# Performance work log

Hardware: AMD Instinct MI355X
Metric: run time of the kernel (lower is better)

## Reference

```python
import jax, jax.numpy as jnp
import numpy as np

EMBED = 256
HEADS = 8
LEVELS = 3
POINTS = 4
MLP = 4
SS = np.array([[100, 100], [50, 50], [25, 25]], np.int32)  # (H, W) per level


def setup_inputs() -> dict:
    key = jax.random.key(0)
    ks = jax.random.split(key, 12)
    B, Q = 2, 128 * 128
    NV = int((SS[:, 0] * SS[:, 1]).sum())
    C = EMBED
    F = C * MLP
    s = 0.02

    def w(k, shape):
        return jax.random.normal(k, shape, jnp.float32) * s

    return dict(
        query=jax.random.normal(ks[0], (B, Q, C), jnp.float32),
        value=jax.random.normal(ks[1], (B, NV, C), jnp.float32),
        query_pos=jax.random.normal(ks[2], (B, Q, C), jnp.float32),
        ref_pts=jax.random.uniform(ks[3], (B, Q, 2), jnp.float32),
        spatial_shapes=SS,
        level_start_index=np.concatenate([[0], np.cumsum(SS[:, 0] * SS[:, 1])[:-1]]).astype(np.int32),
        ln1_g=jnp.ones(C), ln1_b=jnp.zeros(C),
        ln2_g=jnp.ones(C), ln2_b=jnp.zeros(C),
        W_value=w(ks[4], (C, C)), b_value=jnp.zeros(C),
        W_off=w(ks[5], (C, HEADS * LEVELS * POINTS * 2)), b_off=w(ks[6], (HEADS * LEVELS * POINTS * 2,)),
        W_attn=w(ks[7], (C, HEADS * LEVELS * POINTS)), b_attn=jnp.zeros(HEADS * LEVELS * POINTS),
        W_out=w(ks[8], (C, C)), b_out=jnp.zeros(C),
        W_ffn1=w(ks[9], (C, F)), b_ffn1=jnp.zeros(F),
        W_ffn2=w(ks[10], (F, C)), b_ffn2=jnp.zeros(C),
    )


def _layernorm(x, g, b, eps=1e-5):
    m = x.mean(-1, keepdims=True)
    v = ((x - m) ** 2).mean(-1, keepdims=True)
    return (x - m) * jax.lax.rsqrt(v + eps) * g + b


def _bilinear(v, loc, Hl, Wl):
    # v: [BH, Hl*Wl, d]; loc: [BH, Q, P, 2] normalized to [0,1].
    # grid_sample(align_corners=False, padding=zeros): pixel = loc*size - 0.5
    BH, Q, P, _ = loc.shape
    d = v.shape[-1]
    x = loc[..., 0] * Wl - 0.5
    y = loc[..., 1] * Hl - 0.5
    x0f = jnp.floor(x)
    y0f = jnp.floor(y)
    lx = x - x0f
    ly = y - y0f
    x0 = x0f.astype(jnp.int32)
    y0 = y0f.astype(jnp.int32)

    def gather(xi, yi):
        valid = ((xi >= 0) & (xi < Wl) & (yi >= 0) & (yi < Hl)).astype(v.dtype)
        idx = jnp.clip(yi, 0, Hl - 1) * Wl + jnp.clip(xi, 0, Wl - 1)
        g = jnp.take_along_axis(v, idx.reshape(BH, Q * P, 1), axis=1).reshape(BH, Q, P, d)
        return g * valid[..., None]

    w00 = (1 - lx) * (1 - ly)
    w01 = lx * (1 - ly)
    w10 = (1 - lx) * ly
    w11 = lx * ly
    return (gather(x0, y0) * w00[..., None] + gather(x0 + 1, y0) * w01[..., None]
            + gather(x0, y0 + 1) * w10[..., None] + gather(x0 + 1, y0 + 1) * w11[..., None])


def _forward(query, value, query_pos, ref_pts, spatial_shapes,
             ln1_g, ln1_b, ln2_g, ln2_b,
             W_value, b_value, W_off, b_off, W_attn, b_attn, W_out, b_out,
             W_ffn1, b_ffn1, W_ffn2, b_ffn2):
    B, Q, C = query.shape
    Hh, L, P = HEADS, LEVELS, POINTS
    d = C // Hh
    ss = np.asarray(spatial_shapes)
    starts = np.concatenate([[0], np.cumsum(ss[:, 0] * ss[:, 1])])

    # pre-norm + positional embedding (MSDeformAttn adds query_pos)
    qn = _layernorm(query, ln1_g, ln1_b)
    q = qn + query_pos

    # value projection, split heads
    v = (value @ W_value + b_value).reshape(B, -1, Hh, d)

    off = (q @ W_off + b_off).reshape(B, Q, Hh, L, P, 2)
    aw = jax.nn.softmax((q @ W_attn + b_attn).reshape(B, Q, Hh, L * P), axis=-1)
    aw = aw.reshape(B, Q, Hh, L, P)

    # offset normalizer is (W, H) per level
    normalizer = jnp.asarray(ss[:, ::-1].copy(), jnp.float32)
    # bev_value path: ref_pts broadcast over levels
    loc = ref_pts[:, :, None, None, None, :] + off / normalizer[None, None, None, :, None, :]

    out = jnp.zeros((B * Hh, Q, d), query.dtype)
    for l in range(L):
        Hl, Wl = int(ss[l, 0]), int(ss[l, 1])
        v_l = v[:, starts[l]:starts[l + 1]].transpose(0, 2, 1, 3).reshape(B * Hh, Hl * Wl, d)
        loc_l = loc[:, :, :, l].transpose(0, 2, 1, 3, 4).reshape(B * Hh, Q, P, 2)
        sampled = _bilinear(v_l, loc_l, Hl, Wl)  # [BH, Q, P, d]
        w_l = aw[:, :, :, l].transpose(0, 2, 1, 3).reshape(B * Hh, Q, P)
        out = out + (sampled * w_l[..., None]).sum(2)

    out = out.reshape(B, Hh, Q, d).transpose(0, 2, 1, 3).reshape(B, Q, C)
    x = query + (out @ W_out + b_out)

    h = _layernorm(x, ln2_g, ln2_b)
    x = x + (jax.nn.gelu(h @ W_ffn1 + b_ffn1, approximate=False) @ W_ffn2 + b_ffn2)
    return x


def reference(query, value, query_pos, ref_pts, spatial_shapes, level_start_index,
              ln1_g, ln1_b, ln2_g, ln2_b,
              W_value, b_value, W_off, b_off, W_attn, b_attn, W_out, b_out,
              W_ffn1, b_ffn1, W_ffn2, b_ffn2):
    return _forward(query, value, query_pos, ref_pts, spatial_shapes,
                    ln1_g, ln1_b, ln2_g, ln2_b,
                    W_value, b_value, W_off, b_off, W_attn, b_attn, W_out, b_out,
                    W_ffn1, b_ffn1, W_ffn2, b_ffn2)
```

## Files before the change

### kernel.cpp

```cpp
#include <hip/hip_runtime.h>
#include <hip/hip_bf16.h>

#define BQ      2
#define QLEN    16384
#define CDIM    256
#define HEADS   8
#define LEV     3
#define PTS     4
#define DHEAD   32
#define NVTOT   13125
#define FDIM    1024
#define NTOK    (BQ*QLEN)
#define MROWS_V (BQ*NVTOT)
#define NPROJ   288

typedef __attribute__((ext_vector_type(8))) short short8;
typedef __attribute__((ext_vector_type(4))) float floatx4;

typedef const __attribute__((address_space(1))) unsigned int gu32;
typedef __attribute__((address_space(3))) unsigned int lu32;

struct bf16x4 { __hip_bfloat16 v[4]; };

__device__ __forceinline__ int imin(int a, int b){ return a<b?a:b; }
__device__ __forceinline__ int imax(int a, int b){ return a>b?a:b; }

__device__ __forceinline__ float gelu_f(float x)
{
    float u = 0.7978845608028654f * (x + 0.044715f * x * x * x);
    float e = __expf(2.0f * u);
    float th = 1.0f - 2.0f / (e + 1.0f);
    return 0.5f * x * (1.0f + th);
}

__global__ __launch_bounds__(256)
void ln_bf16_k(const float* __restrict__ x, const float* __restrict__ pos,
               const float* __restrict__ g, const float* __restrict__ b,
               __hip_bfloat16* __restrict__ out)
{
    int tok  = blockIdx.x * 4 + (threadIdx.x >> 6);
    int lane = threadIdx.x & 63;
    float4 v = ((const float4*)(x + (size_t)tok * CDIM))[lane];
    float s = v.x + v.y + v.z + v.w;
    #pragma unroll
    for (int o = 32; o > 0; o >>= 1) s += __shfl_down(s, o);
    s = __shfl(s, 0);
    float mean = s * (1.0f / 256.0f);
    float4 c; c.x = v.x - mean; c.y = v.y - mean; c.z = v.z - mean; c.w = v.w - mean;
    float q2 = c.x*c.x + c.y*c.y + c.z*c.z + c.w*c.w;
    #pragma unroll
    for (int o = 32; o > 0; o >>= 1) q2 += __shfl_down(q2, o);
    q2 = __shfl(q2, 0);
    float rstd = rsqrtf(q2 * (1.0f / 256.0f) + 1e-5f);
    float4 gg = ((const float4*)g)[lane];
    float4 bb = ((const float4*)b)[lane];
    float4 o4;
    o4.x = c.x * rstd * gg.x + bb.x;
    o4.y = c.y * rstd * gg.y + bb.y;
    o4.z = c.z * rstd * gg.z + bb.z;
    o4.w = c.w * rstd * gg.w + bb.w;
    if (pos) {
        float4 p = ((const float4*)(pos + (size_t)tok * CDIM))[lane];
        o4.x += p.x; o4.y += p.y; o4.z += p.z; o4.w += p.w;
    }
    bf16x4 r;
    r.v[0] = __float2bfloat16(o4.x); r.v[1] = __float2bfloat16(o4.y);
    r.v[2] = __float2bfloat16(o4.z); r.v[3] = __float2bfloat16(o4.w);
    ((bf16x4*)(out + (size_t)tok * CDIM))[lane] = r;
}

__global__ __launch_bounds__(256)
void cvt_k(const float* __restrict__ in, __hip_bfloat16* __restrict__ out, int n4)
{
    int i = blockIdx.x * 256 + threadIdx.x;
    if (i >= n4) return;
    float4 v = ((const float4*)in)[i];
    bf16x4 r;
    r.v[0] = __float2bfloat16(v.x); r.v[1] = __float2bfloat16(v.y);
    r.v[2] = __float2bfloat16(v.z); r.v[3] = __float2bfloat16(v.w);
    ((bf16x4*)out)[i] = r;
}

__global__ __launch_bounds__(256)
void wt_all_k(const float* __restrict__ Wv,  const float* __restrict__ Woff,
              const float* __restrict__ Wat, const float* __restrict__ Wout,
              const float* __restrict__ W1,  const float* __restrict__ W2,
              const float* __restrict__ boff, const float* __restrict__ bat,
              __hip_bfloat16* __restrict__ o_v,  __hip_bfloat16* __restrict__ o_c,
              __hip_bfloat16* __restrict__ o_out,
              __hip_bfloat16* __restrict__ o_1,  __hip_bfloat16* __restrict__ o_2,
              float* __restrict__ o_bc)
{
    int gid = blockIdx.x * 256 + threadIdx.x;
    if (gid < 65536) {
        int idx = gid, n = idx >> 8, k = idx & 255;
        o_v[idx] = __float2bfloat16(Wv[(size_t)k * 256 + n]);
    } else if (gid < 163840) {
        int idx = gid - 65536, n = idx >> 8, k = idx & 255;
        float v = 0.0f;
        if (n < 192)       v = Woff[(size_t)k * 192 + n];
        else if (n < 288)  v = Wat[(size_t)k * 96 + (n - 192)];
        o_c[idx] = __float2bfloat16(v);
    } else if (gid < 229376) {
        int idx = gid - 163840, n = idx >> 8, k = idx & 255;
        o_out[idx] = __float2bfloat16(Wout[(size_t)k * 256 + n]);
    } else if (gid < 491520) {
        int idx = gid - 229376, n = idx >> 8, k = idx & 255;
        o_1[idx] = __float2bfloat16(W1[(size_t)k * 1024 + n]);
    } else if (gid < 753664) {
        int idx = gid - 491520, n = idx >> 10, k = idx & 1023;
        o_2[idx] = __float2bfloat16(W2[(size_t)k * 256 + n]);
    } else if (gid < 753952) {
        int idx = gid - 753664;
        o_bc[idx] = (idx < 192) ? boff[idx] : bat[idx - 192];
    }
}

enum { EP_PLAIN = 0, EP_VSCAT_BF16 = 1, EP_RES = 2, EP_GELU_BF16 = 3 };

__global__ __launch_bounds__(256)
void mm_k(const __hip_bfloat16* __restrict__ A, const __hip_bfloat16* __restrict__ Bt,
          const float* __restrict__ bias, const float* __restrict__ res,
          void* __restrict__ Cout, int M, int N, int K, int mode)
{
    __shared__ __hip_bfloat16 Ws[128 * 64];
    __shared__ __hip_bfloat16 Ts[128 * 64];
    int t = threadIdx.x;
    int lane = t & 63;
    int wave = t >> 6;
    int wm = wave >> 1, wn = wave & 1;
    int lm = lane & 15, lk = lane >> 4;
    int m0 = blockIdx.x * 128;
    int n0 = blockIdx.y * 128;

    floatx4 acc[4][4];
    #pragma unroll
    for (int i = 0; i < 4; i++)
        #pragma unroll
        for (int j = 0; j < 4; j++) acc[i][j] = (floatx4)0.0f;

    for (int kt = 0; kt < K; kt += 64) {
        #pragma unroll
        for (int i = 0; i < 4; i++) {
            int cc  = i * 256 + t;
            int row = cc >> 3;
            int c   = cc & 7;
            int kc  = c ^ (row & 7);
            int ra  = m0 + row; if (ra >= M) ra = M - 1;
            const __hip_bfloat16* gw = Bt + (size_t)(n0 + row) * K + kt + kc * 8;
            const __hip_bfloat16* gt = A  + (size_t)ra * K + kt + kc * 8;
            __builtin_amdgcn_global_load_lds((gu32*)gw, (lu32*)(Ws + cc * 8), 16, 0, 0);
            __builtin_amdgcn_global_load_lds((gu32*)gt, (lu32*)(Ts + cc * 8), 16, 0, 0);
        }
        __syncthreads();
        #pragma unroll
        for (int ks = 0; ks < 2; ks++) {
            short8 wf[4], tf[4];
            #pragma unroll
            for (int i = 0; i < 4; i++) {
                int rw = wn * 64 + i * 16 + lm;
                int cw = (ks * 4 + lk) ^ (rw & 7);
                wf[i] = *(const short8*)(Ws + (rw * 8 + cw) * 8);
                int rt = wm * 64 + i * 16 + lm;
                int ct = (ks * 4 + lk) ^ (rt & 7);
                tf[i] = *(const short8*)(Ts + (rt * 8 + ct) * 8);
            }
            #pragma unroll
            for (int i = 0; i < 4; i++)
                #pragma unroll
                for (int j = 0; j < 4; j++)
                    acc[i][j] = __builtin_amdgcn_mfma_f32_16x16x32_bf16(wf[i], tf[j], acc[i][j], 0, 0, 0);
        }
        __syncthreads();
    }

    #pragma unroll
    for (int i = 0; i < 4; i++) {
        int chan = n0 + wn * 64 + i * 16 + lk * 4;
        float4 b4 = make_float4(0.f, 0.f, 0.f, 0.f);
        if (chan < N) b4 = *(const float4*)(bias + chan);
        #pragma unroll
        for (int j = 0; j < 4; j++) {
            int tok = m0 + wm * 64 + j * 16 + lm;
            if (tok >= M || chan >= N) continue;
            float4 v;
            v.x = acc[i][j][0] + b4.x;
            v.y = acc[i][j][1] + b4.y;
            v.z = acc[i][j][2] + b4.z;
            v.w = acc[i][j][3] + b4.w;
            if (mode == EP_PLAIN) {
                *(float4*)((float*)Cout + (size_t)tok * N + chan) = v;
            } else if (mode == EP_VSCAT_BF16) {
                int bb  = tok / NVTOT;
                int pix = tok - bb * NVTOT;
                int hh  = chan >> 5, dc = chan & 31;
                bf16x4 r;
                r.v[0] = __float2bfloat16(v.x); r.v[1] = __float2bfloat16(v.y);
                r.v[2] = __float2bfloat16(v.z); r.v[3] = __float2bfloat16(v.w);
                *(bf16x4*)((__hip_bfloat16*)Cout
                    + (((size_t)(bb * HEADS + hh)) * NVTOT + pix) * DHEAD + dc) = r;
            } else if (mode == EP_RES) {
                float4 rr = *(const float4*)(res + (size_t)tok * N + chan);
                v.x += rr.x; v.y += rr.y; v.z += rr.z; v.w += rr.w;
                *(float4*)((float*)Cout + (size_t)tok * N + chan) = v;
            } else {
                bf16x4 r;
                r.v[0] = __float2bfloat16(gelu_f(v.x));
                r.v[1] = __float2bfloat16(gelu_f(v.y));
                r.v[2] = __float2bfloat16(gelu_f(v.z));
                r.v[3] = __float2bfloat16(gelu_f(v.w));
                *(bf16x4*)((__hip_bfloat16*)Cout + (size_t)tok * N + chan) = r;
            }
        }
    }
}

__global__ __launch_bounds__(256)
void sample_k(const __hip_bfloat16* __restrict__ v, const float* __restrict__ cbuf,
              const float* __restrict__ ref, __hip_bfloat16* __restrict__ out)
{
    __shared__ int4   metaIdx[4 * 104];
    __shared__ float4 metaW[4 * 104];

    int wid  = threadIdx.x >> 6;
    int lane = threadIdx.x & 63;
    int t    = blockIdx.x * 4 + wid;
    int b    = t >> 14;
    float rx = ref[(size_t)t * 2 + 0];
    float ry = ref[(size_t)t * 2 + 1];
    const float* crow = cbuf + (size_t)t * NPROJ;

    #pragma unroll
    for (int rnd = 0; rnd < 2; rnd++) {
        int slot = rnd * 64 + lane;
        int h = slot >> 4, p = slot & 15;
        int pc = imin(p, 11);
        float2 oxy  = *(const float2*)(crow + h * 24 + pc * 2);
        float logit = crow[192 + h * 12 + pc];
        float mx = logit;
        #pragma unroll
        for (int o = 8; o > 0; o >>= 1) mx = fmaxf(mx, __shfl_xor(mx, o, 16));
        float e = (p < 12) ? __expf(logit - mx) : 0.0f;
        float ssum = e;
        #pragma unroll
        for (int o = 8; o > 0; o >>= 1) ssum += __shfl_xor(ssum, o, 16);
        float aw = e / ssum;

        if (p < 12) {
            int l = p >> 2;
            float fS = (l == 0) ? 100.0f : ((l == 1) ? 50.0f : 25.0f);
            int   Wl = (l == 0) ? 100 : ((l == 1) ? 50 : 25);
            int   st = (l == 0) ? 0 : ((l == 1) ? 10000 : 12500);
            float x = (rx + oxy.x / fS) * fS - 0.5f;
            float y = (ry + oxy.y / fS) * fS - 0.5f;
            float x0f = floorf(x), y0f = floorf(y);
            float fx = x - x0f, fy = y - y0f;
            int x0 = (int)x0f, y0 = (int)y0f;
            int x1 = x0 + 1,  y1 = y0 + 1;
            int cx0 = imin(imax(x0, 0), Wl - 1), cx1 = imin(imax(x1, 0), Wl - 1);
            int cy0 = imin(imax(y0, 0), Wl - 1), cy1 = imin(imax(y1, 0), Wl - 1);
            float vx0 = (x0 >= 0 && x0 < Wl) ? 1.0f : 0.0f;
            float vx1 = (x1 >= 0 && x1 < Wl) ? 1.0f : 0.0f;
            float vy0 = (y0 >= 0 && y0 < Wl) ? 1.0f : 0.0f;
            float vy1 = (y1 >= 0 && y1 < Wl) ? 1.0f : 0.0f;
            int s = wid * 104 + h * 13 + p;
            metaIdx[s] = make_int4(st + cy0 * Wl + cx0, st + cy0 * Wl + cx1,
                                   st + cy1 * Wl + cx0, st + cy1 * Wl + cx1);
            metaW[s] = make_float4((1.0f - fx) * (1.0f - fy) * aw * vx0 * vy0,
                                   fx * (1.0f - fy) * aw * vx1 * vy0,
                                   (1.0f - fx) * fy * aw * vx0 * vy1,
                                   fx * fy * aw * vx1 * vy1);
        }
    }
    __syncthreads();

    int h  = lane >> 3;
    int c8 = lane & 7;
    const __hip_bfloat16* vbh = v + ((size_t)(b * HEADS + h)) * NVTOT * DHEAD + c8 * 4;
    float4 acc = {0.0f, 0.0f, 0.0f, 0.0f};
    #pragma unroll
    for (int p = 0; p < 12; p++) {
        int s = wid * 104 + h * 13 + p;
        int4   mi = metaIdx[s];
        float4 mw = metaW[s];
        ushort4 r0 = *(const ushort4*)(vbh + (size_t)mi.x * DHEAD);
        ushort4 r1 = *(const ushort4*)(vbh + (size_t)mi.y * DHEAD);
        ushort4 r2 = *(const ushort4*)(vbh + (size_t)mi.z * DHEAD);
        ushort4 r3 = *(const ushort4*)(vbh + (size_t)mi.w * DHEAD);
        acc.x = fmaf(mw.x, __uint_as_float((unsigned)r0.x << 16), acc.x);
        acc.y = fmaf(mw.x, __uint_as_float((unsigned)r0.y << 16), acc.y);
        acc.z = fmaf(mw.x, __uint_as_float((unsigned)r0.z << 16), acc.z);
        acc.w = fmaf(mw.x, __uint_as_float((unsigned)r0.w << 16), acc.w);
        acc.x = fmaf(mw.y, __uint_as_float((unsigned)r1.x << 16), acc.x);
        acc.y = fmaf(mw.y, __uint_as_float((unsigned)r1.y << 16), acc.y);
        acc.z = fmaf(mw.y, __uint_as_float((unsigned)r1.z << 16), acc.z);
        acc.w = fmaf(mw.y, __uint_as_float((unsigned)r1.w << 16), acc.w);
        acc.x = fmaf(mw.z, __uint_as_float((unsigned)r2.x << 16), acc.x);
        acc.y = fmaf(mw.z, __uint_as_float((unsigned)r2.y << 16), acc.y);
        acc.z = fmaf(mw.z, __uint_as_float((unsigned)r2.z << 16), acc.z);
        acc.w = fmaf(mw.z, __uint_as_float((unsigned)r2.w << 16), acc.w);
        acc.x = fmaf(mw.w, __uint_as_float((unsigned)r3.x << 16), acc.x);
        acc.y = fmaf(mw.w, __uint_as_float((unsigned)r3.y << 16), acc.y);
        acc.z = fmaf(mw.w, __uint_as_float((unsigned)r3.z << 16), acc.z);
        acc.w = fmaf(mw.w, __uint_as_float((unsigned)r3.w << 16), acc.w);
    }
    bf16x4 r;
    r.v[0] = __float2bfloat16(acc.x); r.v[1] = __float2bfloat16(acc.y);
    r.v[2] = __float2bfloat16(acc.z); r.v[3] = __float2bfloat16(acc.w);
    *(bf16x4*)(out + (size_t)t * CDIM + h * DHEAD + c8 * 4) = r;
}

extern "C" void kernel_launch(void* const* d_in, const int* in_sizes, int n_in,
                              void* d_out, int out_size, void* d_ws, size_t ws_size,
                              hipStream_t stream)
{
    const float* query = (const float*)d_in[0];
    const float* value = (const float*)d_in[1];
    const float* qpos  = (const float*)d_in[2];
    const float* ref   = (const float*)d_in[3];
    const float* ln1g  = (const float*)d_in[6];
    const float* ln1b  = (const float*)d_in[7];
    const float* ln2g  = (const float*)d_in[8];
    const float* ln2b  = (const float*)d_in[9];
    const float* Wv    = (const float*)d_in[10];
    const float* bv    = (const float*)d_in[11];
    const float* Woff  = (const float*)d_in[12];
    const float* boff  = (const float*)d_in[13];
    const float* Wat   = (const float*)d_in[14];
    const float* bat   = (const float*)d_in[15];
    const float* Wout  = (const float*)d_in[16];
    const float* bout  = (const float*)d_in[17];
    const float* W1    = (const float*)d_in[18];
    const float* b1    = (const float*)d_in[19];
    const float* W2    = (const float*)d_in[20];
    const float* b2    = (const float*)d_in[21];
    float* out = (float*)d_out;
    char*  ws  = (char*)d_ws;

    const size_t MB = 1024 * 1024;
    __hip_bfloat16* Wvt   = (__hip_bfloat16*)(ws + 0);
    __hip_bfloat16* Wct   = (__hip_bfloat16*)(ws + 131072);
    __hip_bfloat16* Woutt = (__hip_bfloat16*)(ws + 327680);
    __hip_bfloat16* W1t   = (__hip_bfloat16*)(ws + 458752);
    __hip_bfloat16* W2t   = (__hip_bfloat16*)(ws + 983040);
    float*          bcomb = (float*)(ws + 1507328);
    __hip_bfloat16* qbf   = (__hip_bfloat16*)(ws + 2  * MB);
    __hip_bfloat16* aoutb = (__hip_bfloat16*)(ws + 19 * MB);
    __hip_bfloat16* vbf   = (__hip_bfloat16*)(ws + 36 * MB);
    __hip_bfloat16* vbuf  = (__hip_bfloat16*)(ws + 50 * MB);
    float*          cbuf  = (float*)(ws + 77 * MB);
    __hip_bfloat16* gbf   = (__hip_bfloat16*)(ws + 50 * MB);
    __hip_bfloat16* hbf   = qbf;

    wt_all_k<<<2946, 256, 0, stream>>>(Wv, Woff, Wat, Wout, W1, W2, boff, bat,
                                       Wvt, Wct, Woutt, W1t, W2t, bcomb);
    cvt_k<<<(MROWS_V * CDIM / 4 + 255) / 256, 256, 0, stream>>>(value, vbf, MROWS_V * CDIM / 4);
    ln_bf16_k<<<NTOK / 4, 256, 0, stream>>>(query, qpos, ln1g, ln1b, qbf);
    mm_k<<<dim3((MROWS_V + 127) / 128, 2), 256, 0, stream>>>(
        vbf, Wvt, bv, nullptr, vbuf, MROWS_V, 256, 256, EP_VSCAT_BF16);
    mm_k<<<dim3(NTOK / 128, 3), 256, 0, stream>>>(
        qbf, Wct, bcomb, nullptr, cbuf, NTOK, NPROJ, 256, EP_PLAIN);
    sample_k<<<NTOK / 4, 256, 0, stream>>>(vbuf, cbuf, ref, aoutb);
    mm_k<<<dim3(NTOK / 128, 2), 256, 0, stream>>>(
        aoutb, Woutt, bout, query, out, NTOK, 256, 256, EP_RES);
    ln_bf16_k<<<NTOK / 4, 256, 0, stream>>>(out, nullptr, ln2g, ln2b, hbf);
    mm_k<<<dim3(NTOK / 128, 8), 256, 0, stream>>>(
        hbf, W1t, b1, nullptr, gbf, NTOK, FDIM, 256, EP_GELU_BF16);
    mm_k<<<dim3(NTOK / 128, 2), 256, 0, stream>>>(
        gbf, W2t, b2, out, out, NTOK, 256, FDIM, EP_RES);
}
```

Baseline: 403.6 us.

## Stage GEMM epilogue through shared memory and store offset/attn projections as bf16

Rewrites the GEMM epilogue so each wave writes bias-added accumulators as packed bf16 into swizzled shared memory, after which threads read back row-contiguous chunks and issue coalesced 8-byte global stores. The offset/attention projection output is now stored in bf16 instead of fp32, which halves that buffer's traffic into the sampling kernel. The GELU buffer moves to a separate workspace region. Rounding every GEMM output to bf16 before the residual add and before GELU loses precision, and the extra shared-memory round trip adds a barrier.

```diff
diff --git a/kernel.cpp b/kernel.cpp
--- a/kernel.cpp
+++ b/kernel.cpp
@@ -24,6 +24,30 @@
 
 __device__ __forceinline__ int imin(int a, int b){ return a<b?a:b; }
 __device__ __forceinline__ int imax(int a, int b){ return a>b?a:b; }
+
+__device__ __forceinline__ float bf2f(unsigned short u){ return __uint_as_float((unsigned)u << 16); }
+__device__ __forceinline__ unsigned short f2bf(float f)
+{
+    __hip_bfloat16 h = __float2bfloat16(f);
+    return *(unsigned short*)&h;
+}
+__device__ __forceinline__ unsigned long long pack4(float4 v)
+{
+    unsigned long long r = (unsigned long long)f2bf(v.x)
+                         | ((unsigned long long)f2bf(v.y) << 16)
+                         | ((unsigned long long)f2bf(v.z) << 32)
+                         | ((unsigned long long)f2bf(v.w) << 48);
+    return r;
+}
+__device__ __forceinline__ float4 unpack4(unsigned long long c)
+{
+    float4 v;
+    v.x = bf2f((unsigned short)(c));
+    v.y = bf2f((unsigned short)(c >> 16));
+    v.z = bf2f((unsigned short)(c >> 32));
+    v.w = bf2f((unsigned short)(c >> 48));
+    return v;
+}
 
 __device__ __forceinline__ float gelu_f(float x)
 {
@@ -63,10 +87,7 @@
         float4 p = ((const float4*)(pos + (size_t)tok * CDIM))[lane];
         o4.x += p.x; o4.y += p.y; o4.z += p.z; o4.w += p.w;
     }
-    bf16x4 r;
-    r.v[0] = __float2bfloat16(o4.x); r.v[1] = __float2bfloat16(o4.y);
-    r.v[2] = __float2bfloat16(o4.z); r.v[3] = __float2bfloat16(o4.w);
-    ((bf16x4*)(out + (size_t)tok * CDIM))[lane] = r;
+    *(unsigned long long*)(out + (size_t)tok * CDIM + lane * 4) = pack4(o4);
 }
 
 __global__ __launch_bounds__(256)
@@ -75,10 +96,7 @@
     int i = blockIdx.x * 256 + threadIdx.x;
     if (i >= n4) return;
     float4 v = ((const float4*)in)[i];
-    bf16x4 r;
-    r.v[0] = __float2bfloat16(v.x); r.v[1] = __float2bfloat16(v.y);
-    r.v[2] = __float2bfloat16(v.z); r.v[3] = __float2bfloat16(v.w);
-    ((bf16x4*)out)[i] = r;
+    *(unsigned long long*)(out + (size_t)i * 4) = pack4(v);
 }
 
 __global__ __launch_bounds__(256)
@@ -116,15 +134,17 @@
     }
 }
 
-enum { EP_PLAIN = 0, EP_VSCAT_BF16 = 1, EP_RES = 2, EP_GELU_BF16 = 3 };
+enum { EP_PLAIN_BF16 = 0, EP_VSCAT_BF16 = 1, EP_RES = 2, EP_GELU_BF16 = 3 };
 
 __global__ __launch_bounds__(256)
 void mm_k(const __hip_bfloat16* __restrict__ A, const __hip_bfloat16* __restrict__ Bt,
           const float* __restrict__ bias, const float* __restrict__ res,
           void* __restrict__ Cout, int M, int N, int K, int mode)
 {
-    __shared__ __hip_bfloat16 Ws[128 * 64];
-    __shared__ __hip_bfloat16 Ts[128 * 64];
+    __shared__ float4 smem4[2048];
+    __hip_bfloat16* Ws = (__hip_bfloat16*)smem4;
+    __hip_bfloat16* Ts = (__hip_bfloat16*)smem4 + 128*64;
+    unsigned long long* st = (unsigned long long*)smem4;
     int t = threadIdx.x;
     int lane = t & 63;
     int wave = t >> 6;
@@ -179,44 +199,52 @@
         int chan = n0 + wn * 64 + i * 16 + lk * 4;
         float4 b4 = make_float4(0.f, 0.f, 0.f, 0.f);
         if (chan < N) b4 = *(const float4*)(bias + chan);
+        int c4 = wn * 16 + i * 4 + lk;
         #pragma unroll
         for (int j = 0; j < 4; j++) {
-            int tok = m0 + wm * 64 + j * 16 + lm;
-            if (tok >= M || chan >= N) continue;
+            int tl = wm * 64 + j * 16 + lm;
             float4 v;
             v.x = acc[i][j][0] + b4.x;
             v.y = acc[i][j][1] + b4.y;
             v.z = acc[i][j][2] + b4.z;
             v.w = acc[i][j][3] + b4.w;
-            if (mode == EP_PLAIN) {
-                *(float4*)((float*)Cout + (size_t)tok * N + chan) = v;
-            } else if (mode == EP_VSCAT_BF16) {
-                int bb  = tok / NVTOT;
-                int pix = tok - bb * NVTOT;
-                int hh  = chan >> 5, dc = chan & 31;
-                bf16x4 r;
-                r.v[0] = __float2bfloat16(v.x); r.v[1] = __float2bfloat16(v.y);
-                r.v[2] = __float2bfloat16(v.z); r.v[3] = __float2bfloat16(v.w);
-                *(bf16x4*)((__hip_bfloat16*)Cout
-                    + (((size_t)(bb * HEADS + hh)) * NVTOT + pix) * DHEAD + dc) = r;
-            } else if (mode == EP_RES) {
-                float4 rr = *(const float4*)(res + (size_t)tok * N + chan);
-                v.x += rr.x; v.y += rr.y; v.z += rr.z; v.w += rr.w;
-                *(float4*)((float*)Cout + (size_t)tok * N + chan) = v;
-            } else {
-                bf16x4 r;
-                r.v[0] = __float2bfloat16(gelu_f(v.x));
-                r.v[1] = __float2bfloat16(gelu_f(v.y));
-                r.v[2] = __float2bfloat16(gelu_f(v.z));
-                r.v[3] = __float2bfloat16(gelu_f(v.w));
-                *(bf16x4*)((__hip_bfloat16*)Cout + (size_t)tok * N + chan) = r;
-            }
-        }
-    }
-}
-
-__global__ __launch_bounds__(256)
-void sample_k(const __hip_bfloat16* __restrict__ v, const float* __restrict__ cbuf,
+            st[tl * 32 + (c4 ^ (tl & 31))] = pack4(v);
+        }
+    }
+    __syncthreads();
+
+    int rel  = (t & 31) * 4;
+    int c4r  = t & 31;
+    #pragma unroll
+    for (int it = 0; it < 16; it++) {
+        int tl   = it * 8 + (t >> 5);
+        int tok  = m0 + tl;
+        int chan = n0 + rel;
+        if (tok >= M || chan >= N) continue;
+        unsigned long long chunk = st[tl * 32 + (c4r ^ (tl & 31))];
+        if (mode == EP_PLAIN_BF16) {
+            *(unsigned long long*)((__hip_bfloat16*)Cout + (size_t)tok * N + chan) = chunk;
+        } else if (mode == EP_VSCAT_BF16) {
+            int bb  = tok / NVTOT;
+            int pix = tok - bb * NVTOT;
+            int hd  = chan >> 5, dc = chan & 31;
+            *(unsigned long long*)((__hip_bfloat16*)Cout
+                + (((size_t)(bb * HEADS + hd)) * NVTOT + pix) * DHEAD + dc) = chunk;
+        } else if (mode == EP_GELU_BF16) {
+            float4 v = unpack4(chunk);
+            v.x = gelu_f(v.x); v.y = gelu_f(v.y); v.z = gelu_f(v.z); v.w = gelu_f(v.w);
+            *(unsigned long long*)((__hip_bfloat16*)Cout + (size_t)tok * N + chan) = pack4(v);
+        } else {
+            float4 v = unpack4(chunk);
+            float4 rr = *(const float4*)(res + (size_t)tok * N + chan);
+            v.x += rr.x; v.y += rr.y; v.z += rr.z; v.w += rr.w;
+            *(float4*)((float*)Cout + (size_t)tok * N + chan) = v;
+        }
+    }
+}
+
+__global__ __launch_bounds__(256)
+void sample_k(const __hip_bfloat16* __restrict__ v, const __hip_bfloat16* __restrict__ cbuf,
               const float* __restrict__ ref, __hip_bfloat16* __restrict__ out)
 {
     __shared__ int4   metaIdx[4 * 104];
@@ -228,15 +256,17 @@
     int b    = t >> 14;
     float rx = ref[(size_t)t * 2 + 0];
     float ry = ref[(size_t)t * 2 + 1];
-    const float* crow = cbuf + (size_t)t * NPROJ;
+    const __hip_bfloat16* crow = cbuf + (size_t)t * NPROJ;
 
     #pragma unroll
     for (int rnd = 0; rnd < 2; rnd++) {
         int slot = rnd * 64 + lane;
         int h = slot >> 4, p = slot & 15;
         int pc = imin(p, 11);
-        float2 oxy  = *(const float2*)(crow + h * 24 + pc * 2);
-        float logit = crow[192 + h * 12 + pc];
+        unsigned upk = *(const unsigned*)(crow + h * 24 + pc * 2);
+        float ox = bf2f((unsigned short)upk);
+        float oy = bf2f((unsigned short)(upk >> 16));
+        float logit = bf2f(*(const unsigned short*)(crow + 192 + h * 12 + pc));
         float mx = logit;
         #pragma unroll
         for (int o = 8; o > 0; o >>= 1) mx = fmaxf(mx, __shfl_xor(mx, o, 16));
@@ -251,8 +281,8 @@
             float fS = (l == 0) ? 100.0f : ((l == 1) ? 50.0f : 25.0f);
             int   Wl = (l == 0) ? 100 : ((l == 1) ? 50 : 25);
             int   st = (l == 0) ? 0 : ((l == 1) ? 10000 : 12500);
-            float x = (rx + oxy.x / fS) * fS - 0.5f;
-            float y = (ry + oxy.y / fS) * fS - 0.5f;
+            float x = (rx + ox / fS) * fS - 0.5f;
+            float y = (ry + oy / fS) * fS - 0.5f;
             float x0f = floorf(x), y0f = floorf(y);
             float fx = x - x0f, fy = y - y0f;
             int x0 = (int)x0f, y0 = (int)y0f;
@@ -287,27 +317,24 @@
         ushort4 r1 = *(const ushort4*)(vbh + (size_t)mi.y * DHEAD);
         ushort4 r2 = *(const ushort4*)(vbh + (size_t)mi.z * DHEAD);
         ushort4 r3 = *(const ushort4*)(vbh + (size_t)mi.w * DHEAD);
-        acc.x = fmaf(mw.x, __uint_as_float((unsigned)r0.x << 16), acc.x);
-        acc.y = fmaf(mw.x, __uint_as_float((unsigned)r0.y << 16), acc.y);
-        acc.z = fmaf(mw.x, __uint_as_float((unsigned)r0.z << 16), acc.z);
-        acc.w = fmaf(mw.x, __uint_as_float((unsigned)r0.w << 16), acc.w);
-        acc.x = fmaf(mw.y, __uint_as_float((unsigned)r1.x << 16), acc.x);
-        acc.y = fmaf(mw.y, __uint_as_float((unsigned)r1.y << 16), acc.y);
-        acc.z = fmaf(mw.y, __uint_as_float((unsigned)r1.z << 16), acc.z);
-        acc.w = fmaf(mw.y, __uint_as_float((unsigned)r1.w << 16), acc.w);
-        acc.x = fmaf(mw.z, __uint_as_float((unsigned)r2.x << 16), acc.x);
-        acc.y = fmaf(mw.z, __uint_as_float((unsigned)r2.y << 16), acc.y);
-        acc.z = fmaf(mw.z, __uint_as_float((unsigned)r2.z << 16), acc.z);
-        acc.w = fmaf(mw.z, __uint_as_float((unsigned)r2.w << 16), acc.w);
-        acc.x = fmaf(mw.w, __uint_as_float((unsigned)r3.x << 16), acc.x);
-        acc.y = fmaf(mw.w, __uint_as_float((unsigned)r3.y << 16), acc.y);
-        acc.z = fmaf(mw.w, __uint_as_float((unsigned)r3.z << 16), acc.z);
-        acc.w = fmaf(mw.w, __uint_as_float((unsigned)r3.w << 16), acc.w);
-    }
-    bf16x4 r;
-    r.v[0] = __float2bfloat16(acc.x); r.v[1] = __float2bfloat16(acc.y);
-    r.v[2] = __float2bfloat16(acc.z); r.v[3] = __float2bfloat16(acc.w);
-    *(bf16x4*)(out + (size_t)t * CDIM + h * DHEAD + c8 * 4) = r;
+        acc.x = fmaf(mw.x, bf2f(r0.x), acc.x);
+        acc.y = fmaf(mw.x, bf2f(r0.y), acc.y);
+        acc.z = fmaf(mw.x, bf2f(r0.z), acc.z);
+        acc.w = fmaf(mw.x, bf2f(r0.w), acc.w);
+        acc.x = fmaf(mw.y, bf2f(r1.x), acc.x);
+        acc.y = fmaf(mw.y, bf2f(r1.y), acc.y);
+        acc.z = fmaf(mw.y, bf2f(r1.z), acc.z);
+        acc.w = fmaf(mw.y, bf2f(r1.w), acc.w);
+        acc.x = fmaf(mw.z, bf2f(r2.x), acc.x);
+        acc.y = fmaf(mw.z, bf2f(r2.y), acc.y);
+        acc.z = fmaf(mw.z, bf2f(r2.z), acc.z);
+        acc.w = fmaf(mw.z, bf2f(r2.w), acc.w);
+        acc.x = fmaf(mw.w, bf2f(r3.x), acc.x);
+        acc.y = fmaf(mw.w, bf2f(r3.y), acc.y);
+        acc.z = fmaf(mw.w, bf2f(r3.z), acc.z);
+        acc.w = fmaf(mw.w, bf2f(r3.w), acc.w);
+    }
+    *(unsigned long long*)(out + (size_t)t * CDIM + h * DHEAD + c8 * 4) = pack4(acc);
 }
 
 extern "C" void kernel_launch(void* const* d_in, const int* in_sizes, int n_in,
@@ -348,8 +375,8 @@
     __hip_bfloat16* aoutb = (__hip_bfloat16*)(ws + 19 * MB);
     __hip_bfloat16* vbf   = (__hip_bfloat16*)(ws + 36 * MB);
     __hip_bfloat16* vbuf  = (__hip_bfloat16*)(ws + 50 * MB);
-    float*          cbuf  = (float*)(ws + 77 * MB);
-    __hip_bfloat16* gbf   = (__hip_bfloat16*)(ws + 50 * MB);
+    __hip_bfloat16* cbuf  = (__hip_bfloat16*)(ws + 77 * MB);
+    __hip_bfloat16* gbf   = (__hip_bfloat16*)(ws + 100 * MB);
     __hip_bfloat16* hbf   = qbf;
 
     wt_all_k<<<2946, 256, 0, stream>>>(Wv, Woff, Wat, Wout, W1, W2, boff, bat,
@@ -359,7 +386,7 @@
     mm_k<<<dim3((MROWS_V + 127) / 128, 2), 256, 0, stream>>>(
         vbf, Wvt, bv, nullptr, vbuf, MROWS_V, 256, 256, EP_VSCAT_BF16);
     mm_k<<<dim3(NTOK / 128, 3), 256, 0, stream>>>(
-        qbf, Wct, bcomb, nullptr, cbuf, NTOK, NPROJ, 256, EP_PLAIN);
+        qbf, Wct, bcomb, nullptr, cbuf, NTOK, NPROJ, 256, EP_PLAIN_BF16);
     sample_k<<<NTOK / 4, 256, 0, stream>>>(vbuf, cbuf, ref, aoutb);
     mm_k<<<dim3(NTOK / 128, 2), 256, 0, stream>>>(
         aoutb, Woutt, bout, query, out, NTOK, 256, 256, EP_RES);
```

Measured after the change: 367.6 us. 1.1x faster.
